# Kernel tuning notes

Hardware: AMD Instinct MI355X
Metric: run time of the kernel (lower is better)

## Reference

```python
import jax, jax.numpy as jnp
import numpy as np

DIM = 256; K = 3; PAD = 1; DIL = 1; B = 16; H = 56; W = 56
SP = 8           # share_planes
RADIX = 2
ATTN = max(DIM * RADIX // 4, 32)   # 128
EMB = K * K * DIM // SP            # 288

def conv(x, w, pad=0, dil=1, groups=1):
    return jax.lax.conv_general_dilated(
        x, w, (1, 1), [(pad, pad), (pad, pad)], rhs_dilation=(dil, dil),
        feature_group_count=groups, dimension_numbers=('NCHW', 'OIHW', 'NCHW'))

def bn(x, g, b, m, v, eps=1e-5):
    # eval-mode BatchNorm2d
    s = g * jax.lax.rsqrt(v + eps)
    return x * s[None, :, None, None] + (b - m * s)[None, :, None, None]

def gn(x, g, b, groups, eps=1e-5):
    Bb, C, Hh, Ww = x.shape
    xg = x.reshape(Bb, groups, C // groups, Hh, Ww)
    mu = xg.mean((2, 3, 4), keepdims=True)
    var = xg.var((2, 3, 4), keepdims=True)
    xg = (xg - mu) * jax.lax.rsqrt(var + eps)
    return xg.reshape(Bb, C, Hh, Ww) * g[None, :, None, None] + b[None, :, None, None]

def unfold3(x):
    # im2col for 3x3, stride 1, pad 1 -> (B, C, K*K, H, W)
    Bb, C, Hh, Ww = x.shape
    p = (K - 1) // 2
    xp = jnp.pad(x, ((0, 0), (0, 0), (p, p), (p, p)))
    return jnp.stack([xp[:, :, i:i + Hh, j:j + Ww] for i in range(K) for j in range(K)], axis=2)

def reference(x, ke_w, ke_g, ke_b, ke_m, ke_v, e1_w, e1_g, e1_b, e1_m, e1_v,
              e2_w, e2_b, gng, gnb, c1_w, c1_g, c1_b, c1_m, c1_v,
              b2_g, b2_b, b2_m, b2_v, s1_w, s1_b, s1_g, s1_bb, s1_m, s1_v,
              s2_w, s2_b):
    Bb = x.shape[0]
    # key embed: grouped kxk conv + BN + ReLU
    k = jax.nn.relu(bn(conv(x, ke_w, pad=PAD, dil=DIL, groups=4), ke_g, ke_b, ke_m, ke_v))
    qk = jnp.concatenate([x, k], axis=1)                     # (B, 2*DIM, H, W)
    # dynamic kernel branch
    wemb = jax.nn.relu(bn(conv(qk, e1_w), e1_g, e1_b, e1_m, e1_v))
    wemb = conv(wemb, e2_w) + e2_b[None, :, None, None]
    wemb = gn(wemb, gng, gnb, DIM // SP)                     # GroupNorm(dim//8 groups)
    wemb = wemb.reshape(Bb, DIM // SP, K * K, H, W)
    # value branch
    xq = bn(conv(x, c1_w), c1_g, c1_b, c1_m, c1_v)
    # local dynamic convolution: per-pixel kernel shared across SP channels
    patches = unfold3(xq).reshape(Bb, DIM // SP, SP, K * K, H, W)
    y = (patches * wemb[:, :, None]).sum(3).reshape(Bb, DIM, H, W)
    y = bn(y, b2_g, b2_b, b2_m, b2_v)
    y = y * jax.nn.sigmoid(y)                                # swish
    # split attention over radix=2 branches (y, k)
    xs = jnp.stack([y, k], axis=2)                           # (B, C, 2, H, W)
    gap = xs.sum(2).mean((2, 3), keepdims=True)              # (B, C, 1, 1)
    a = jax.nn.relu(bn(conv(gap, s1_w) + s1_b[None, :, None, None], s1_g, s1_bb, s1_m, s1_v))
    a = conv(a, s2_w) + s2_b[None, :, None, None]            # (B, 2*C, 1, 1)
    a = jax.nn.softmax(a.reshape(Bb, DIM, RADIX), axis=2)
    out = (xs * a[:, :, :, None, None]).sum(2)
    return out

def setup_inputs():
    key = jax.random.key(0)
    ks = iter(jax.random.split(key, 40))
    def n(shape, s=1.0):
        return jax.random.normal(next(ks), shape, jnp.float32) * s
    def u(shape):
        return jax.random.uniform(next(ks), shape, jnp.float32, minval=0.5, maxval=1.5)
    d = {}
    d['x'] = n((B, DIM, H, W))
    d['ke_w'] = n((DIM, DIM // 4, K, K), 0.05)
    d['ke_g'] = u((DIM,)); d['ke_b'] = n((DIM,), 0.1); d['ke_m'] = n((DIM,), 0.1); d['ke_v'] = u((DIM,))
    d['e1_w'] = n((DIM // 2, 2 * DIM, 1, 1), 0.05)
    d['e1_g'] = u((DIM // 2,)); d['e1_b'] = n((DIM // 2,), 0.1); d['e1_m'] = n((DIM // 2,), 0.1); d['e1_v'] = u((DIM // 2,))
    d['e2_w'] = n((EMB, DIM // 2, 1, 1), 0.05); d['e2_b'] = n((EMB,), 0.1)
    d['gng'] = u((EMB,)); d['gnb'] = n((EMB,), 0.1)
    d['c1_w'] = n((DIM, DIM, 1, 1), 0.05)
    d['c1_g'] = u((DIM,)); d['c1_b'] = n((DIM,), 0.1); d['c1_m'] = n((DIM,), 0.1); d['c1_v'] = u((DIM,))
    d['b2_g'] = u((DIM,)); d['b2_b'] = n((DIM,), 0.1); d['b2_m'] = n((DIM,), 0.1); d['b2_v'] = u((DIM,))
    d['s1_w'] = n((ATTN, DIM, 1, 1), 0.05); d['s1_b'] = n((ATTN,), 0.1)
    d['s1_g'] = u((ATTN,)); d['s1_bb'] = n((ATTN,), 0.1); d['s1_m'] = n((ATTN,), 0.1); d['s1_v'] = u((ATTN,))
    d['s2_w'] = n((RADIX * DIM, ATTN, 1, 1), 0.05); d['s2_b'] = n((RADIX * DIM,), 0.1)
    return d
```

## Files before the change

### kernel.cpp

```cpp
#include <hip/hip_runtime.h>
#include <hip/hip_bf16.h>

typedef __hip_bfloat16 bf16;
typedef float f32x4 __attribute__((ext_vector_type(4)));
typedef short s16x8 __attribute__((ext_vector_type(8)));

#define NPIX 3136
#define HDIM 56
#define CDIM 256
#define PPIX 3364

static __device__ __forceinline__ float b2f(bf16 v){ return __bfloat162float(v); }
static __device__ __forceinline__ bf16  f2b(float v){ return __float2bfloat16(v); }

#define O_KE_S 0
#define O_KE_B 256
#define O_E1_S 512
#define O_E1_B 640
#define O_C1_S 768
#define O_C1_B 1024
#define O_B2_S 1280
#define O_B2_B 1536
#define O_S1_S 1792
#define O_S1_B 1920
#define O_E2B  2048
#define O_GNS  2336
#define O_GAP  3360
#define O_ATT  7456

__global__ void prep(
    const float* __restrict__ kew, const float* __restrict__ e1w,
    const float* __restrict__ e2w, const float* __restrict__ c1w,
    const float* keg, const float* keb, const float* kem, const float* kev,
    const float* e1g, const float* e1b, const float* e1m, const float* e1v,
    const float* e2b,
    const float* c1g, const float* c1b, const float* c1m, const float* c1v,
    const float* b2g, const float* b2b, const float* b2m, const float* b2v,
    const float* s1g, const float* s1bb, const float* s1m, const float* s1v,
    bf16* kewT, bf16* e1wb, bf16* e2wb, bf16* c1wb, float* o)
{
    int bid = blockIdx.x, t = threadIdx.x;
    if (bid < 576) {
        int i = bid * 256 + t;
        int ci = i & 63, co_l = (i >> 6) & 63;
        int gt = i >> 12;
        int tap = gt % 9, g = gt / 9;
        int co = g * 64 + co_l;
        kewT[i] = f2b(kew[(co * 64 + ci) * 9 + tap]);
    } else if (bid < 832) {
        int i = (bid - 576) * 256 + t; e1wb[i] = f2b(e1w[i]);
    } else if (bid < 976) {
        int i = (bid - 832) * 256 + t; e2wb[i] = f2b(e2w[i]);
    } else if (bid < 1232) {
        int i = (bid - 976) * 256 + t; c1wb[i] = f2b(c1w[i]);
    } else if (bid == 1232) {
        const float eps = 1e-5f;
        {
            float s = keg[t] * rsqrtf(kev[t] + eps);
            o[O_KE_S + t] = s; o[O_KE_B + t] = keb[t] - kem[t] * s;
            s = c1g[t] * rsqrtf(c1v[t] + eps);
            o[O_C1_S + t] = s; o[O_C1_B + t] = c1b[t] - c1m[t] * s;
            s = b2g[t] * rsqrtf(b2v[t] + eps);
            o[O_B2_S + t] = s; o[O_B2_B + t] = b2b[t] - b2m[t] * s;
        }
        if (t < 128) {
            float s = e1g[t] * rsqrtf(e1v[t] + eps);
            o[O_E1_S + t] = s; o[O_E1_B + t] = e1b[t] - e1m[t] * s;
            s = s1g[t] * rsqrtf(s1v[t] + eps);
            o[O_S1_S + t] = s; o[O_S1_B + t] = s1bb[t] - s1m[t] * s;
        }
        for (int i = t; i < 288; i += 256) o[O_E2B + i] = e2b[i];
    } else {
        int j = (bid - 1233) * 256 + t;
        if (j < 1024) o[O_GNS + j] = 0.f;
        else          o[O_GAP + j - 1024] = 0.f;
    }
}

__global__ __launch_bounds__(256) void cvt_x(const float* __restrict__ x, bf16* __restrict__ xh)
{
    int b = blockIdx.y;
    int p0 = blockIdx.x * 64;
    __shared__ bf16 T[64][264];
    int t = threadIdx.x;

    if (blockIdx.x == 0) {
        float4 z = {0.f, 0.f, 0.f, 0.f};
        for (int s = t; s < 7296; s += 256) {
            int pi = s >> 5, cc = s & 31;
            int pos;
            if (pi < 58)       pos = pi;
            else if (pi < 116) pos = 57 * 58 + (pi - 58);
            else if (pi < 172) pos = (pi - 115) * 58;
            else               pos = (pi - 171) * 58 + 57;
            *(float4*)(xh + ((long)b * PPIX + pos) * 256 + cc * 8) = z;
        }
    }

    for (int it = 0; it < 16; it++) {
        int slot = t + it * 256;
        int c = slot >> 4, ch4 = slot & 15;
        float4 v = *(const float4*)(x + ((long)b * CDIM + c) * NPIX + p0 + ch4 * 4);
        T[ch4 * 4 + 0][c] = f2b(v.x);
        T[ch4 * 4 + 1][c] = f2b(v.y);
        T[ch4 * 4 + 2][c] = f2b(v.z);
        T[ch4 * 4 + 3][c] = f2b(v.w);
    }
    __syncthreads();
    for (int it = 0; it < 8; it++) {
        int slot = t + it * 256;
        int p = slot >> 5, cc = slot & 31;
        int pl = p0 + p;
        int h = pl / HDIM, w = pl - h * HDIM;
        *(float4*)(xh + ((long)b * PPIX + (h + 1) * 58 + (w + 1)) * 256 + cc * 8) = *(const float4*)&T[p][cc * 8];
    }
}

__global__ __launch_bounds__(256, 4) void gconv_mfma(
    const bf16* __restrict__ xp, const bf16* __restrict__ wT,
    const float* __restrict__ scale, const float* __restrict__ bias,
    bf16* __restrict__ kh, float* __restrict__ gap)
{
    int b = blockIdx.z, g = blockIdx.y;
    int h0 = blockIdx.x * 2;
    __shared__ bf16 As[232 * 64];
    int t = threadIdx.x;
    int wv = t >> 6, lane = t & 63, q = lane >> 4, ln = lane & 15;

    #pragma unroll
    for (int i = 0; i < 8; i++) {
        int slot = t + i * 256;
        if (slot < 1856) {
            int pos = slot >> 3, chunkL = slot & 7;
            int ri = pos / 58, ci = pos - ri * 58;
            int chunkg = chunkL ^ (pos & 7);
            float4 v = *(const float4*)(xp + (((long)b * PPIX + (h0 + ri) * 58 + ci) * 256 + g * 64 + chunkg * 8));
            *(float4*)&As[pos * 64 + chunkL * 8] = v;
        }
    }

    int posb[7];
    #pragma unroll
    for (int pt = 0; pt < 7; pt++) {
        int p = pt * 16 + ln;
        int prow = (p >= 56) ? 1 : 0;
        int pcol = p - prow * 56;
        posb[pt] = prow * 58 + pcol + 1;
    }
    const bf16* wbase = wT + ((long)(g * 9) * 64 + wv * 16 + ln) * 64;

    __syncthreads();

    f32x4 acc[7] = {};
    #pragma unroll
    for (int tap = 0; tap < 9; tap++) {
        const int dr = tap / 3;
        const int dc = tap % 3 - 1;
        const bf16* wq = wbase + tap * 64 * 64;
        s16x8 B0 = *(const s16x8*)(wq + q * 8);
        s16x8 B1 = *(const s16x8*)(wq + 32 + q * 8);
        #pragma unroll
        for (int pt = 0; pt < 7; pt++) {
            int pos = posb[pt] + dr * 58 + dc;
            int off0 = pos * 64 + ((q ^ (pos & 7)) * 8);
            s16x8 a0 = *(const s16x8*)&As[off0];
            s16x8 a1 = *(const s16x8*)&As[off0 ^ 32];
            acc[pt] = __builtin_amdgcn_mfma_f32_16x16x32_bf16(a0, B0, acc[pt], 0, 0, 0);
            acc[pt] = __builtin_amdgcn_mfma_f32_16x16x32_bf16(a1, B1, acc[pt], 0, 0, 0);
        }
    }

    __syncthreads();
    bf16* T = As;
    int co = g * 64 + wv * 16 + ln;
    float sc = scale[co], bi = bias[co];
    #pragma unroll
    for (int pt = 0; pt < 7; pt++)
        #pragma unroll
        for (int r = 0; r < 4; r++)
            T[(pt * 16 + q * 4 + r) * 72 + wv * 16 + ln] = f2b(fmaxf(acc[pt][r] * sc + bi, 0.f));
    __syncthreads();
    int pimg0 = blockIdx.x * 112;
    #pragma unroll
    for (int i = 0; i < 4; i++) {
        int slot = t + i * 256;
        if (slot < 896) {
            int row = slot >> 3, cc = slot & 7;
            *(float4*)(kh + ((long)b * NPIX + pimg0 + row) * CDIM + g * 64 + cc * 8) = *(const float4*)&T[row * 72 + cc * 8];
        }
    }
    {
        int co_l = t & 63, rb = t >> 6;
        float s = 0.f;
        #pragma unroll
        for (int r = 0; r < 28; r++) s += b2f(T[(rb * 28 + r) * 72 + co_l]);
        atomicAdd(&gap[b * 256 + g * 64 + co_l], s);
    }
}

__global__ __launch_bounds__(256) void gemm_pair(
    const bf16* __restrict__ e1w, const bf16* __restrict__ c1w,
    const bf16* __restrict__ X0, const bf16* __restrict__ X1,
    const float* __restrict__ fold,
    bf16* __restrict__ Ye1, bf16* __restrict__ Yc1)
{
    int b = blockIdx.z;
    int p0 = blockIdx.x * 64;
    int by = blockIdx.y;
    const bf16* Wt; int K, M, m0; const float *scp, *bip; bf16* Y; bool relu;
    if (by == 0) { Wt = e1w; K = 512; M = 128; m0 = 0;
                   scp = fold + O_E1_S; bip = fold + O_E1_B; Y = Ye1; relu = true; }
    else         { Wt = c1w; K = 256; M = 256; m0 = (by - 1) * 128;
                   scp = fold + O_C1_S; bip = fold + O_C1_B; Y = Yc1; relu = false; }
    const int C0 = 256;

    __shared__ bf16 SH[64 * 72 + 128 * 72];
    bf16* As = SH;
    bf16* Bs = SH + 64 * 72;
    int t = threadIdx.x;
    int wv = t >> 6, lane = t & 63, q = lane >> 4, ln = lane & 15;

    f32x4 acc[4][2] = {};
    for (int k0 = 0; k0 < K; k0 += 64) {
        __syncthreads();
        #pragma unroll
        for (int i = 0; i < 2; i++) {
            int slot = t + i * 256;
            int chunk = slot & 7, row = slot >> 3;
            int ch = k0 + chunk * 8;
            const bf16* src;
            if (ch < C0) {
                long pp = p0 + row;
                long pidx = (long)b * PPIX + pp + 2 * (pp / HDIM) + 59;
                src = X0 + pidx * C0 + ch;
            } else {
                src = X1 + ((long)b * NPIX + p0 + row) * 256 + (ch - C0);
            }
            *(float4*)&As[row * 72 + chunk * 8] = *(const float4*)src;
        }
        #pragma unroll
        for (int i = 0; i < 4; i++) {
            int slot = t + i * 256;
            int chunk = slot & 7, row = slot >> 3;
            *(float4*)&Bs[row * 72 + chunk * 8] = *(const float4*)(Wt + (long)(m0 + row) * K + k0 + chunk * 8);
        }
        __syncthreads();
        #pragma unroll
        for (int kk = 0; kk < 2; kk++) {
            s16x8 a[4];
            #pragma unroll
            for (int pt = 0; pt < 4; pt++)
                a[pt] = *(const s16x8*)&As[(pt * 16 + ln) * 72 + kk * 32 + q * 8];
            #pragma unroll
            for (int mi = 0; mi < 2; mi++) {
                s16x8 bb = *(const s16x8*)&Bs[(wv * 32 + mi * 16 + ln) * 72 + kk * 32 + q * 8];
                #pragma unroll
                for (int pt = 0; pt < 4; pt++)
                    acc[pt][mi] = __builtin_amdgcn_mfma_f32_16x16x32_bf16(a[pt], bb, acc[pt][mi], 0, 0, 0);
            }
        }
    }

    __syncthreads();
    bf16* T = SH;
    #pragma unroll
    for (int mi = 0; mi < 2; mi++) {
        int m = m0 + wv * 32 + mi * 16 + ln;
        float sc = scp[m], bi = bip[m];
        #pragma unroll
        for (int pt = 0; pt < 4; pt++) {
            #pragma unroll
            for (int r = 0; r < 4; r++) {
                float v = acc[pt][mi][r] * sc + bi;
                if (relu) v = fmaxf(v, 0.f);
                T[(pt * 16 + q * 4 + r) * 144 + wv * 32 + mi * 16 + ln] = f2b(v);
            }
        }
    }
    __syncthreads();
    int nst = (M == 128) ? 2 : 4;
    for (int i = 0; i < nst; i++) {
        int slot = t + i * 256;
        int chunk = slot & (2 * (M / 128) * 8 - 1), row = slot / (2 * (M / 128) * 8);
        ;
    }
    {
        int chunks = M / 8;
        int total = 64 * chunks;
        for (int slot = t; slot < total; slot += 256) {
            int row = slot / chunks, chunk = slot - row * chunks;
            int m = m0 + chunk * 8;
            if (m < m0 + 128)
                *(float4*)(Y + ((long)b * NPIX + p0 + row) * M + m) = *(const float4*)&T[row * 144 + chunk * 8];
        }
    }
}

__global__ __launch_bounds__(256) void mfma_gemm_e2(
    const bf16* __restrict__ Wt, const bf16* __restrict__ X0,
    const float* __restrict__ bias,
    bf16* __restrict__ Y, float* __restrict__ gnsum)
{
    const int K = 128, M = 288;
    int b = blockIdx.z;
    int p0 = blockIdx.x * 64;
    int m0 = blockIdx.y * 128;
    __shared__ bf16 SH[64 * 72 + 128 * 72];
    bf16* As = SH;
    bf16* Bs = SH + 64 * 72;
    __shared__ float gs[64];
    int t = threadIdx.x;
    int wv = t >> 6, lane = t & 63, q = lane >> 4, ln = lane & 15;
    if (t < 64) gs[t] = 0.f;

    f32x4 acc[4][2] = {};
    for (int k0 = 0; k0 < K; k0 += 64) {
        __syncthreads();
        #pragma unroll
        for (int i = 0; i < 2; i++) {
            int slot = t + i * 256;
            int chunk = slot & 7, row = slot >> 3;
            int ch = k0 + chunk * 8;
            *(float4*)&As[row * 72 + chunk * 8] = *(const float4*)(X0 + ((long)b * NPIX + p0 + row) * K + ch);
        }
        #pragma unroll
        for (int i = 0; i < 4; i++) {
            int slot = t + i * 256;
            int chunk = slot & 7, row = slot >> 3;
            int m = m0 + row;
            float4 v = {0.f, 0.f, 0.f, 0.f};
            if (m < M) v = *(const float4*)(Wt + (long)m * K + k0 + chunk * 8);
            *(float4*)&Bs[row * 72 + chunk * 8] = v;
        }
        __syncthreads();
        #pragma unroll
        for (int kk = 0; kk < 2; kk++) {
            s16x8 a[4];
            #pragma unroll
            for (int pt = 0; pt < 4; pt++)
                a[pt] = *(const s16x8*)&As[(pt * 16 + ln) * 72 + kk * 32 + q * 8];
            #pragma unroll
            for (int mi = 0; mi < 2; mi++) {
                s16x8 bb = *(const s16x8*)&Bs[(wv * 32 + mi * 16 + ln) * 72 + kk * 32 + q * 8];
                #pragma unroll
                for (int pt = 0; pt < 4; pt++)
                    acc[pt][mi] = __builtin_amdgcn_mfma_f32_16x16x32_bf16(a[pt], bb, acc[pt][mi], 0, 0, 0);
            }
        }
    }

    __syncthreads();
    bf16* T = SH;
    #pragma unroll
    for (int mi = 0; mi < 2; mi++) {
        int m = m0 + wv * 32 + mi * 16 + ln;
        int mc = (m > M - 1) ? (M - 1) : m;
        float bi = bias[mc];
        float ps = 0.f, pq = 0.f;
        #pragma unroll
        for (int pt = 0; pt < 4; pt++) {
            #pragma unroll
            for (int r = 0; r < 4; r++) {
                float v = acc[pt][mi][r] + bi;
                ps += v; pq += v * v;
                T[(pt * 16 + q * 4 + r) * 144 + wv * 32 + mi * 16 + ln] = f2b(v);
            }
        }
        if (m < M) {
            int grp = m / 9;
            atomicAdd(&gs[grp * 2], ps);
            atomicAdd(&gs[grp * 2 + 1], pq);
        }
    }
    __syncthreads();
    #pragma unroll
    for (int i = 0; i < 4; i++) {
        int slot = t + i * 256;
        int chunk = slot & 15, row = slot >> 4;
        int m = m0 + chunk * 8;
        if (m + 8 <= M)
            *(float4*)(Y + ((long)b * NPIX + p0 + row) * M + m) = *(const float4*)&T[row * 144 + chunk * 8];
    }
    if (t < 64) atomicAdd(&gnsum[b * 64 + t], gs[t]);
}

__global__ __launch_bounds__(256) void dynconv(
    const bf16* __restrict__ xq, const bf16* __restrict__ wemb,
    const float* __restrict__ gnsum,
    const float* __restrict__ gng, const float* __restrict__ gnb,
    const float* __restrict__ b2s, const float* __restrict__ b2b,
    bf16* __restrict__ y, float* __restrict__ gap)
{
    int id = blockIdx.x * 256 + threadIdx.x;
    int grp = id & 31;
    int p = (id >> 5) % NPIX;
    int b = id / (NPIX * 32);
    int h = p / HDIM, w = p % HDIM;
    float S = gnsum[b * 64 + grp * 2], Q = gnsum[b * 64 + grp * 2 + 1];
    float mu = S * (1.f / 28224.f);
    float var = Q * (1.f / 28224.f) - mu * mu;
    float rs = rsqrtf(fmaxf(var, 0.f) + 1e-5f);
    const bf16* wp = wemb + ((long)b * NPIX + p) * 288 + grp * 9;
    float wv[9];
    #pragma unroll
    for (int tp = 0; tp < 9; tp++)
        wv[tp] = (b2f(wp[tp]) - mu) * rs * gng[grp * 9 + tp] + gnb[grp * 9 + tp];
    float acc[8] = {};
    #pragma unroll
    for (int tp = 0; tp < 9; tp++) {
        int h2 = h + tp / 3 - 1, w2 = w + tp % 3 - 1;
        if ((unsigned)h2 >= HDIM || (unsigned)w2 >= HDIM) continue;
        const bf16* xp = xq + ((long)b * NPIX + h2 * HDIM + w2) * CDIM + grp * 8;
        s16x8 xv = *(const s16x8*)xp;
        const bf16* xb = (const bf16*)&xv;
        float wt = wv[tp];
        #pragma unroll
        for (int i = 0; i < 8; i++) acc[i] += b2f(xb[i]) * wt;
    }
    bf16 outv[8];
    float sv[8];
    #pragma unroll
    for (int i = 0; i < 8; i++) {
        int c = grp * 8 + i;
        float v = acc[i] * b2s[c] + b2b[c];
        float sw = v / (1.f + __expf(-v));
        sv[i] = sw;
        outv[i] = f2b(sw);
    }
    *(float4*)(y + ((long)b * NPIX + p) * CDIM + grp * 8) = *(const float4*)outv;

    __shared__ float R[8][256];
    int pl = threadIdx.x >> 5;
    #pragma unroll
    for (int i = 0; i < 8; i++) R[pl][grp * 8 + i] = sv[i];
    __syncthreads();
    float s = 0.f;
    #pragma unroll
    for (int j = 0; j < 8; j++) s += R[j][threadIdx.x];
    atomicAdd(&gap[b * 256 + threadIdx.x], s);
}

__global__ void attnk(const float* __restrict__ gap,
                      const float* __restrict__ s1w, const float* __restrict__ s1b,
                      const float* __restrict__ s1s, const float* __restrict__ s1bi,
                      const float* __restrict__ s2w, const float* __restrict__ s2b,
                      float* __restrict__ att)
{
    int b = blockIdx.x, t = threadIdx.x;
    __shared__ float g[256], a1[128];
    for (int i = t; i < 256; i += 128) g[i] = gap[b * 256 + i] * (1.f / NPIX);
    __syncthreads();
    float s = 0.f;
    for (int ci = 0; ci < 256; ci++) s += s1w[t * 256 + ci] * g[ci];
    s += s1b[t];
    s = s * s1s[t] + s1bi[t];
    a1[t] = fmaxf(s, 0.f);
    __syncthreads();
    for (int c = t; c < 256; c += 128) {
        float v0 = s2b[2 * c], v1 = s2b[2 * c + 1];
        for (int ci = 0; ci < 128; ci++) {
            float av = a1[ci];
            v0 += s2w[(2 * c) * 128 + ci] * av;
            v1 += s2w[(2 * c + 1) * 128 + ci] * av;
        }
        float m = fmaxf(v0, v1);
        float e0 = __expf(v0 - m), e1 = __expf(v1 - m);
        float inv = 1.f / (e0 + e1);
        att[(b * 256 + c) * 2 + 0] = e0 * inv;
        att[(b * 256 + c) * 2 + 1] = e1 * inv;
    }
}

__global__ __launch_bounds__(256) void finalk(
    const bf16* __restrict__ y, const bf16* __restrict__ k,
    const float* __restrict__ att, float* __restrict__ out)
{
    int b = blockIdx.z, c0 = blockIdx.y * 64, p0 = blockIdx.x * 64;
    __shared__ bf16 Ys[64][72], Ks[64][72];
    int t = threadIdx.x;
    #pragma unroll
    for (int i = 0; i < 2; i++) {
        int slot = t + i * 256;
        int row = slot >> 3, cc = slot & 7;
        long off = ((long)b * NPIX + p0 + row) * CDIM + c0 + cc * 8;
        *(float4*)&Ys[row][cc * 8] = *(const float4*)(y + off);
        *(float4*)&Ks[row][cc * 8] = *(const float4*)(k + off);
    }
    __syncthreads();
    int c_l = t >> 2, pc = t & 3;
    int c = c0 + c_l;
    float a0 = att[(b * 256 + c) * 2], a1 = att[(b * 256 + c) * 2 + 1];
    float4 o[4];
    float* of = (float*)o;
    #pragma unroll
    for (int j = 0; j < 16; j++) {
        int p = pc * 16 + j;
        of[j] = b2f(Ys[p][c_l]) * a0 + b2f(Ks[p][c_l]) * a1;
    }
    float* dst = out + ((long)b * CDIM + c) * NPIX + p0 + pc * 16;
    #pragma unroll
    for (int j = 0; j < 4; j++) ((float4*)dst)[j] = o[j];
}

extern "C" void kernel_launch(void* const* d_in, const int* in_sizes, int n_in,
                              void* d_out, int out_size, void* d_ws, size_t ws_size,
                              hipStream_t stream)
{
    const float* x    = (const float*)d_in[0];
    const float* ke_w = (const float*)d_in[1];
    const float* ke_g = (const float*)d_in[2];
    const float* ke_b = (const float*)d_in[3];
    const float* ke_m = (const float*)d_in[4];
    const float* ke_v = (const float*)d_in[5];
    const float* e1_w = (const float*)d_in[6];
    const float* e1_g = (const float*)d_in[7];
    const float* e1_b = (const float*)d_in[8];
    const float* e1_m = (const float*)d_in[9];
    const float* e1_v = (const float*)d_in[10];
    const float* e2_w = (const float*)d_in[11];
    const float* e2_b = (const float*)d_in[12];
    const float* gng  = (const float*)d_in[13];
    const float* gnb  = (const float*)d_in[14];
    const float* c1_w = (const float*)d_in[15];
    const float* c1_g = (const float*)d_in[16];
    const float* c1_b = (const float*)d_in[17];
    const float* c1_m = (const float*)d_in[18];
    const float* c1_v = (const float*)d_in[19];
    const float* b2_g = (const float*)d_in[20];
    const float* b2_b = (const float*)d_in[21];
    const float* b2_m = (const float*)d_in[22];
    const float* b2_v = (const float*)d_in[23];
    const float* s1_w = (const float*)d_in[24];
    const float* s1_b = (const float*)d_in[25];
    const float* s1_g = (const float*)d_in[26];
    const float* s1_bb= (const float*)d_in[27];
    const float* s1_m = (const float*)d_in[28];
    const float* s1_v = (const float*)d_in[29];
    const float* s2_w = (const float*)d_in[30];
    const float* s2_b = (const float*)d_in[31];

    float* fold = (float*)d_ws;
    bf16* wsb   = (bf16*)((char*)d_ws + 65536);
    bf16* xh   = wsb;
    bf16* kh   = xh + 13778944L;
    bf16* wemb = kh + 12845056L;
    bf16* w1   = wemb + 14450688L;
    bf16* kewT = w1 + 6422528L;
    bf16* e1wb = kewT + 147456L;
    bf16* e2wb = e1wb + 65536L;
    bf16* c1wb = e2wb + 36864L;
    bf16* xq   = c1wb + 65536L;
    bf16* yb   = xh;

    prep<<<dim3(1253), dim3(256), 0, stream>>>(
        ke_w, e1_w, e2_w, c1_w,
        ke_g, ke_b, ke_m, ke_v, e1_g, e1_b, e1_m, e1_v, e2_b,
        c1_g, c1_b, c1_m, c1_v, b2_g, b2_b, b2_m, b2_v,
        s1_g, s1_bb, s1_m, s1_v,
        kewT, e1wb, e2wb, c1wb, fold);

    cvt_x<<<dim3(49, 16), dim3(256), 0, stream>>>(x, xh);

    gconv_mfma<<<dim3(28, 4, 16), dim3(256), 0, stream>>>(
        xh, kewT, fold + O_KE_S, fold + O_KE_B, kh, fold + O_GAP);

    gemm_pair<<<dim3(49, 3, 16), dim3(256), 0, stream>>>(
        e1wb, c1wb, xh, kh, fold, w1, xq);

    mfma_gemm_e2<<<dim3(49, 3, 16), dim3(256), 0, stream>>>(
        e2wb, w1, fold + O_E2B, wemb, fold + O_GNS);

    dynconv<<<dim3(6272), dim3(256), 0, stream>>>(
        xq, wemb, fold + O_GNS, gng, gnb,
        fold + O_B2_S, fold + O_B2_B, yb, fold + O_GAP);

    attnk<<<dim3(16), dim3(128), 0, stream>>>(
        fold + O_GAP, s1_w, s1_b, fold + O_S1_S, fold + O_S1_B, s2_w, s2_b, fold + O_ATT);

    finalk<<<dim3(49, 4, 16), dim3(256), 0, stream>>>(yb, kh, fold + O_ATT, (float*)d_out);
}
```

Measured before the change: 351.2 us.

## Write xq into zero-padded layout and stage wemb/GN params in shared memory

The value-branch GEMM now writes xq into a halo-padded 58x58 layout, and cvt_x zeroes its border. This lets dynconv load all nine neighbour vectors unconditionally, with no bounds checks. dynconv also loads its 8-pixel block of wemb into shared memory with vector loads and precomputes the GroupNorm scale and shift per channel in shared memory, removing per-thread strided bf16 loads and repeated GN arithmetic. The cost is extra border writes in cvt_x and one extra block-level sync; the xq buffer must be large enough to hold the padded layout.

```diff
diff --git a/kernel.cpp b/kernel.cpp
--- a/kernel.cpp
+++ b/kernel.cpp
@@ -77,7 +77,8 @@
     }
 }
 
-__global__ __launch_bounds__(256) void cvt_x(const float* __restrict__ x, bf16* __restrict__ xh)
+__global__ __launch_bounds__(256) void cvt_x(const float* __restrict__ x,
+                                             bf16* __restrict__ xh, bf16* __restrict__ xq)
 {
     int b = blockIdx.y;
     int p0 = blockIdx.x * 64;
@@ -94,6 +95,7 @@
             else if (pi < 172) pos = (pi - 115) * 58;
             else               pos = (pi - 171) * 58 + 57;
             *(float4*)(xh + ((long)b * PPIX + pos) * 256 + cc * 8) = z;
+            *(float4*)(xq + ((long)b * PPIX + pos) * 256 + cc * 8) = z;
         }
     }
 
@@ -278,21 +280,14 @@
         }
     }
     __syncthreads();
-    int nst = (M == 128) ? 2 : 4;
-    for (int i = 0; i < nst; i++) {
+    #pragma unroll
+    for (int i = 0; i < 4; i++) {
         int slot = t + i * 256;
-        int chunk = slot & (2 * (M / 128) * 8 - 1), row = slot / (2 * (M / 128) * 8);
-        ;
-    }
-    {
-        int chunks = M / 8;
-        int total = 64 * chunks;
-        for (int slot = t; slot < total; slot += 256) {
-            int row = slot / chunks, chunk = slot - row * chunks;
-            int m = m0 + chunk * 8;
-            if (m < m0 + 128)
-                *(float4*)(Y + ((long)b * NPIX + p0 + row) * M + m) = *(const float4*)&T[row * 144 + chunk * 8];
-        }
+        int row = slot >> 4, chunk = slot & 15;
+        long pp = p0 + row;
+        long pidx = (by == 0) ? ((long)b * NPIX + pp)
+                              : ((long)b * PPIX + pp + 2 * (pp / HDIM) + 59);
+        *(float4*)(Y + pidx * M + m0 + chunk * 8) = *(const float4*)&T[row * 144 + chunk * 8];
     }
 }
 
@@ -391,32 +386,57 @@
     const float* __restrict__ b2s, const float* __restrict__ b2b,
     bf16* __restrict__ y, float* __restrict__ gap)
 {
-    int id = blockIdx.x * 256 + threadIdx.x;
-    int grp = id & 31;
-    int p = (id >> 5) % NPIX;
-    int b = id / (NPIX * 32);
-    int h = p / HDIM, w = p % HDIM;
-    float S = gnsum[b * 64 + grp * 2], Q = gnsum[b * 64 + grp * 2 + 1];
-    float mu = S * (1.f / 28224.f);
-    float var = Q * (1.f / 28224.f) - mu * mu;
-    float rs = rsqrtf(fmaxf(var, 0.f) + 1e-5f);
-    const bf16* wp = wemb + ((long)b * NPIX + p) * 288 + grp * 9;
-    float wv[9];
-    #pragma unroll
-    for (int tp = 0; tp < 9; tp++)
-        wv[tp] = (b2f(wp[tp]) - mu) * rs * gng[grp * 9 + tp] + gnb[grp * 9 + tp];
+    int t = threadIdx.x;
+    int grp = t & 31, pl = t >> 5;
+    int bid = blockIdx.x;
+    int b = bid / 392;
+    int p0 = (bid - b * 392) * 8;
+    int p = p0 + pl;
+    int h = p / HDIM, w = p - h * HDIM;
+
+    __shared__ bf16 WE[2304];
+    __shared__ float SA[288], SC[288];
+    __shared__ float R[8][256];
+
+    {
+        const bf16* src = wemb + (long)(b * NPIX + p0) * 288;
+        #pragma unroll
+        for (int i = 0; i < 2; i++) {
+            int s = t + i * 256;
+            if (s < 288) *(float4*)&WE[s * 8] = *(const float4*)(src + s * 8);
+        }
+    }
+    for (int s = t; s < 288; s += 256) {
+        int g2 = s / 9;
+        float S = gnsum[b * 64 + g2 * 2], Q = gnsum[b * 64 + g2 * 2 + 1];
+        float mu = S * (1.f / 28224.f);
+        float var = Q * (1.f / 28224.f) - mu * mu;
+        float rs = rsqrtf(fmaxf(var, 0.f) + 1e-5f);
+        float a = rs * gng[s];
+        SA[s] = a;
+        SC[s] = gnb[s] - mu * a;
+    }
+    __syncthreads();
+
+    long base = ((long)b * PPIX + (h + 1) * 58 + (w + 1)) * 256 + grp * 8;
+    const bf16* rm = xq + base - 58 * 256;
+    const bf16* rc = xq + base;
+    const bf16* rq = xq + base + 58 * 256;
+    s16x8 xv[9];
+    xv[0] = *(const s16x8*)(rm - 256); xv[1] = *(const s16x8*)rm; xv[2] = *(const s16x8*)(rm + 256);
+    xv[3] = *(const s16x8*)(rc - 256); xv[4] = *(const s16x8*)rc; xv[5] = *(const s16x8*)(rc + 256);
+    xv[6] = *(const s16x8*)(rq - 256); xv[7] = *(const s16x8*)rq; xv[8] = *(const s16x8*)(rq + 256);
+
     float acc[8] = {};
     #pragma unroll
     for (int tp = 0; tp < 9; tp++) {
-        int h2 = h + tp / 3 - 1, w2 = w + tp % 3 - 1;
-        if ((unsigned)h2 >= HDIM || (unsigned)w2 >= HDIM) continue;
-        const bf16* xp = xq + ((long)b * NPIX + h2 * HDIM + w2) * CDIM + grp * 8;
-        s16x8 xv = *(const s16x8*)xp;
-        const bf16* xb = (const bf16*)&xv;
-        float wt = wv[tp];
+        int wi = grp * 9 + tp;
+        float wt = b2f(WE[pl * 288 + wi]) * SA[wi] + SC[wi];
+        const bf16* xb = (const bf16*)&xv[tp];
         #pragma unroll
         for (int i = 0; i < 8; i++) acc[i] += b2f(xb[i]) * wt;
     }
+
     bf16 outv[8];
     float sv[8];
     #pragma unroll
@@ -429,15 +449,13 @@
     }
     *(float4*)(y + ((long)b * NPIX + p) * CDIM + grp * 8) = *(const float4*)outv;
 
-    __shared__ float R[8][256];
-    int pl = threadIdx.x >> 5;
     #pragma unroll
     for (int i = 0; i < 8; i++) R[pl][grp * 8 + i] = sv[i];
     __syncthreads();
     float s = 0.f;
     #pragma unroll
-    for (int j = 0; j < 8; j++) s += R[j][threadIdx.x];
-    atomicAdd(&gap[b * 256 + threadIdx.x], s);
+    for (int j = 0; j < 8; j++) s += R[j][t];
+    atomicAdd(&gap[b * 256 + t], s);
 }
 
 __global__ void attnk(const float* __restrict__ gap,
@@ -559,7 +577,7 @@
         s1_g, s1_bb, s1_m, s1_v,
         kewT, e1wb, e2wb, c1wb, fold);
 
-    cvt_x<<<dim3(49, 16), dim3(256), 0, stream>>>(x, xh);
+    cvt_x<<<dim3(49, 16), dim3(256), 0, stream>>>(x, xh, xq);
 
     gconv_mfma<<<dim3(28, 4, 16), dim3(256), 0, stream>>>(
         xh, kewT, fold + O_KE_S, fold + O_KE_B, kh, fold + O_GAP);
```

After: 355.0 us. About the same (+1.1%).
